# Kernel tuning notes

Measured on AMD Instinct MI355X. Metric: run time of the kernel, lower is better.

Reference implementation:

```python
import jax, jax.numpy as jnp
import numpy as np

FP8_E4M3_MAX = 448.0  # max_value for fp8 e4m3fn in the torch module


def _to_fp8_e4m3(x):
    # round-to-nearest fp8 e4m3fn values, represented back in fp32
    return x.astype(jnp.float8_e4m3fn).astype(jnp.float32)


def setup_inputs() -> dict:
    key = jax.random.key(0)
    k1, k2, k3 = jax.random.split(key, 3)
    B, S, K, N = 4, 2048, 4096, 14336
    x = jax.random.normal(k1, (B, S, K), dtype=jnp.float32)
    # per-tensor scales (QParamsLinear enforces per_tensor qscheme for this path)
    weight_scale = jnp.array([0.01], dtype=jnp.float32)
    input_scale = jnp.array([0.02], dtype=jnp.float32)
    # weight stored in real-quantized fp8 form (values are exact e4m3 lattice points)
    w_fp = jax.random.normal(k2, (N, K), dtype=jnp.float32)
    weight_q = _to_fp8_e4m3(jnp.clip(w_fp / weight_scale, -FP8_E4M3_MAX, FP8_E4M3_MAX))
    bias = jax.random.normal(k3, (N,), dtype=jnp.float32)
    return {"x": x, "weight_q": weight_q, "weight_scale": weight_scale,
            "input_scale": input_scale, "bias": bias}


def reference(x, weight_q, weight_scale, input_scale, bias):
    # Quantize activation: divide by per-tensor scale, clamp to fp8 range, cast to e4m3
    qx = jnp.clip(x / input_scale, -FP8_E4M3_MAX, FP8_E4M3_MAX)
    qx = qx.astype(jnp.float8_e4m3fn).astype(x.dtype)
    # scaled_mm: (qx @ weight_q.T) * (input_scale * weight_scale) + bias
    out = jnp.einsum("bsk,nk->bsn", qx, weight_q.astype(x.dtype))
    out = out * (input_scale * weight_scale)[0] + bias
    return out
```

## Files before the change

### kernel.cpp

```cpp
#include <hip/hip_runtime.h>
#include <stdint.h>

typedef float f32x4  __attribute__((ext_vector_type(4)));
typedef float f32x16 __attribute__((ext_vector_type(16)));
typedef int   i32x4  __attribute__((ext_vector_type(4)));
typedef int   i32x8  __attribute__((ext_vector_type(8)));

constexpr int Mdim = 8192;
constexpr int Ndim = 14336;
constexpr int Kdim = 4096;
constexpr int BM = 256, BN = 256, BK = 64;
constexpr int NT = Kdim / BK;
constexpr uint32_t SLOT = 32768;

#define VMCNT(n) asm volatile("s_waitcnt vmcnt(" #n ")" ::: "memory")
#define LGKM(n)  do { asm volatile("s_waitcnt lgkmcnt(" #n ")" ::: "memory"); \
                      __builtin_amdgcn_sched_barrier(0); } while (0)
#define BARRIER() do { asm volatile("" ::: "memory"); \
                       __builtin_amdgcn_s_barrier(); \
                       asm volatile("" ::: "memory"); } while (0)

__device__ __forceinline__ void gload_lds16(const void* g, void* l) {
  __builtin_amdgcn_global_load_lds(
      (const __attribute__((address_space(1))) unsigned int*)g,
      (__attribute__((address_space(3))) unsigned int*)l, 16, 0, 0);
}

__device__ __forceinline__ i32x4 ldsr128(const uint8_t* p) {
  i32x4 r;
  asm volatile("ds_read_b128 %0, %1"
               : "=v"(r)
               : "v"((const __attribute__((address_space(3))) uint8_t*)p));
  return r;
}

__device__ __forceinline__ i32x8 frag(const uint8_t* tile, int row, int kh) {
  const int p0 = (kh * 32) ^ (((row >> 1) & 3) << 4);
  const uint8_t* rp = tile + row * 64;
  i32x4 lo = ldsr128(rp + p0);
  i32x4 hi = ldsr128(rp + (p0 ^ 16));
  return __builtin_shufflevector(lo, hi, 0, 1, 2, 3, 4, 5, 6, 7);
}

__device__ __forceinline__ f32x16 mx(i32x8 a, i32x8 b, f32x16 c) {
  return __builtin_amdgcn_mfma_scale_f32_32x32x64_f8f6f4(
      a, b, c, 0, 0, 0, 0x7f7f7f7f, 0, 0x7f7f7f7f);
}

__global__ void __launch_bounds__(256) quant_fp8_kernel(
    const float* __restrict__ in, uint8_t* __restrict__ out8,
    const float* __restrict__ scale_ptr, long long n)
{
  const float s = scale_ptr ? scale_ptr[0] : 1.0f;
  const long long nch = n >> 3;
  const long long idx = (long long)blockIdx.x * blockDim.x + threadIdx.x;
  const long long stride = (long long)gridDim.x * blockDim.x;
  for (long long c = idx; c < nch; c += stride) {
    f32x4 v0 = *(const f32x4*)(in + c * 8);
    f32x4 v1 = *(const f32x4*)(in + c * 8 + 4);
    float q[8];
#pragma unroll
    for (int j = 0; j < 4; ++j) {
      q[j]     = fminf(fmaxf(v0[j] / s, -448.f), 448.f);
      q[4 + j] = fminf(fmaxf(v1[j] / s, -448.f), 448.f);
    }
    unsigned int w0 = 0, w1 = 0;
    w0 = __builtin_amdgcn_cvt_pk_fp8_f32(q[0], q[1], w0, false);
    w0 = __builtin_amdgcn_cvt_pk_fp8_f32(q[2], q[3], w0, true);
    w1 = __builtin_amdgcn_cvt_pk_fp8_f32(q[4], q[5], w1, false);
    w1 = __builtin_amdgcn_cvt_pk_fp8_f32(q[6], q[7], w1, true);
    uint2 r; r.x = w0; r.y = w1;
    *(uint2*)(out8 + c * 8) = r;
  }
}

__global__ void __launch_bounds__(512, 2) gemm_fp8_kernel(
    const uint8_t* __restrict__ qa, const uint8_t* __restrict__ qb,
    const float* __restrict__ iscale, const float* __restrict__ wscale,
    const float* __restrict__ bias, float* __restrict__ out)
{
  __shared__ uint8_t smem[4 * SLOT];

  const int tid  = threadIdx.x;
  const int wave = tid >> 6;
  const int lane = tid & 63;
  const int wm   = wave >> 2;
  const int wn   = wave & 3;
  const int col  = lane & 31;
  const int kh   = lane >> 5;
  const long long tile_m = (long long)blockIdx.y * BM;
  const long long tile_n = (long long)blockIdx.x * BN;

  const int urow = tid >> 2;
  const int pbs  = tid & 3;
  const int scol = (pbs ^ ((urow >> 1) & 3)) << 4;
  const uint8_t* gA = qa + (tile_m + urow) * Kdim + scol;
  const uint8_t* gB = qb + (tile_n + urow) * Kdim + scol;
  uint8_t* lbase = smem + wave * 1024;

#define STAGE(u, mat, tt, boff)                                            \
  gload_lds16((mat ? gB : gA) + (long long)(u) * 128 * Kdim +              \
                  (long long)(tt) * BK,                                    \
              lbase + (boff) + (mat) * 16384 + (u) * 8192)

  f32x16 acc[4][2] = {};

  const int rowA = wm * 128 + col;
  const int rowB = wn * 64 + col;

#pragma unroll
  for (int tt = 0; tt < 3; ++tt) {
    STAGE(0, 0, tt, (uint32_t)tt * SLOT); STAGE(1, 0, tt, (uint32_t)tt * SLOT);
    STAGE(0, 1, tt, (uint32_t)tt * SLOT); STAGE(1, 1, tt, (uint32_t)tt * SLOT);
  }

  for (int t = 0; t < NT; ++t) {
    const uint8_t* Ab = smem + (uint32_t)(t & 3) * SLOT;
    const uint8_t* Bb = Ab + 16384;

    if (t + 2 < NT)      { VMCNT(8); }
    else if (t + 1 < NT) { VMCNT(4); }
    else                 { VMCNT(0); }
    BARRIER();

    if (t + 3 < NT) {
      const uint32_t bo = (uint32_t)((t + 3) & 3) * SLOT;
      STAGE(0, 0, t + 3, bo); STAGE(1, 0, t + 3, bo);
      STAGE(0, 1, t + 3, bo); STAGE(1, 1, t + 3, bo);
    }

    i32x8 A0 = frag(Ab, rowA +  0, kh);
    i32x8 A1 = frag(Ab, rowA + 32, kh);
    i32x8 B0 = frag(Bb, rowB +  0, kh);
    i32x8 B1 = frag(Bb, rowB + 32, kh);
    i32x8 A2 = frag(Ab, rowA + 64, kh);
    i32x8 A3 = frag(Ab, rowA + 96, kh);

    LGKM(4);
    __builtin_amdgcn_s_setprio(1);
    acc[0][0] = mx(A0, B0, acc[0][0]);  acc[0][1] = mx(A0, B1, acc[0][1]);
    acc[1][0] = mx(A1, B0, acc[1][0]);  acc[1][1] = mx(A1, B1, acc[1][1]);
    __builtin_amdgcn_s_setprio(0);
    LGKM(0);
    __builtin_amdgcn_s_setprio(1);
    acc[2][0] = mx(A2, B0, acc[2][0]);  acc[2][1] = mx(A2, B1, acc[2][1]);
    acc[3][0] = mx(A3, B0, acc[3][0]);  acc[3][1] = mx(A3, B1, acc[3][1]);
    __builtin_amdgcn_s_setprio(0);
  }

  const float alpha = iscale[0] * wscale[0];
  const long long col0 = tile_n + wn * 64 + col;
  const float bv0 = bias[col0];
  const float bv1 = bias[col0 + 32];
#pragma unroll
  for (int m = 0; m < 4; ++m) {
#pragma unroll
    for (int r = 0; r < 16; ++r) {
      const long long row =
          tile_m + wm * 128 + m * 32 + (r & 3) + 8 * (r >> 2) + 4 * kh;
      float* op = out + row * (long long)Ndim + col0;
      op[0]  = acc[m][0][r] * alpha + bv0;
      op[32] = acc[m][1][r] * alpha + bv1;
    }
  }
#undef STAGE
}

extern "C" void kernel_launch(void* const* d_in, const int* in_sizes, int n_in,
                              void* d_out, int out_size, void* d_ws, size_t ws_size,
                              hipStream_t stream) {
  const float* x      = (const float*)d_in[0];
  const float* weight = (const float*)d_in[1];
  const float* wscale = (const float*)d_in[2];
  const float* iscale = (const float*)d_in[3];
  const float* bias   = (const float*)d_in[4];
  float* out = (float*)d_out;

  uint8_t* qx = (uint8_t*)d_ws;
  uint8_t* qw = qx + (long long)Mdim * Kdim;

  const long long nx = (long long)Mdim * Kdim;
  const long long nw = (long long)Ndim * Kdim;

  quant_fp8_kernel<<<4096, 256, 0, stream>>>(x, qx, iscale, nx);
  quant_fp8_kernel<<<4096, 256, 0, stream>>>(weight, qw, nullptr, nw);

  dim3 grid(Ndim / BN, Mdim / BM);
  gemm_fp8_kernel<<<grid, 512, 0, stream>>>(qx, qw, iscale, wscale, bias, out);
}
```

Measured before the change: 570.2 us.

## Pre-swizzle weights into MFMA fragment layout and load B directly to registers

The weight quantization kernel now writes fp8 weights in a layout pre-arranged per MFMA fragment, so the GEMM loads B operands straight from global memory into registers instead of staging them through LDS. Only A goes through LDS now, with BK raised to 128, a double buffer instead of a 4-stage ring, and a new swizzle. The main loop is unrolled by two, with register double-buffering of the B fragments. This removes LDS traffic and capacity for B, but it gives up the deeper prefetch depth (waits on vmcnt(0) every step) and raises register pressure.

```diff
diff --git a/kernel.cpp b/kernel.cpp
--- a/kernel.cpp
+++ b/kernel.cpp
@@ -1,24 +1,26 @@
 #include <hip/hip_runtime.h>
 #include <stdint.h>
 
-typedef float f32x4  __attribute__((ext_vector_type(4)));
-typedef float f32x16 __attribute__((ext_vector_type(16)));
-typedef int   i32x4  __attribute__((ext_vector_type(4)));
-typedef int   i32x8  __attribute__((ext_vector_type(8)));
+typedef float    f32x4  __attribute__((ext_vector_type(4)));
+typedef float    f32x16 __attribute__((ext_vector_type(16)));
+typedef int      i32x4  __attribute__((ext_vector_type(4)));
+typedef int      i32x8  __attribute__((ext_vector_type(8)));
+typedef uint32_t u32x4  __attribute__((ext_vector_type(4)));
 
 constexpr int Mdim = 8192;
 constexpr int Ndim = 14336;
 constexpr int Kdim = 4096;
-constexpr int BM = 256, BN = 256, BK = 64;
+constexpr int BM = 256, BN = 256, BK = 128;
 constexpr int NT = Kdim / BK;
-constexpr uint32_t SLOT = 32768;
-
-#define VMCNT(n) asm volatile("s_waitcnt vmcnt(" #n ")" ::: "memory")
+
+#define VMCNT(n) do { asm volatile("s_waitcnt vmcnt(" #n ")" ::: "memory"); \
+                      __builtin_amdgcn_sched_barrier(0); } while (0)
 #define LGKM(n)  do { asm volatile("s_waitcnt lgkmcnt(" #n ")" ::: "memory"); \
                       __builtin_amdgcn_sched_barrier(0); } while (0)
 #define BARRIER() do { asm volatile("" ::: "memory"); \
                        __builtin_amdgcn_s_barrier(); \
                        asm volatile("" ::: "memory"); } while (0)
+#define KEEP(x)  asm volatile("" :: "v"(x))
 
 __device__ __forceinline__ void gload_lds16(const void* g, void* l) {
   __builtin_amdgcn_global_load_lds(
@@ -34,9 +36,9 @@
   return r;
 }
 
-__device__ __forceinline__ i32x8 frag(const uint8_t* tile, int row, int kh) {
-  const int p0 = (kh * 32) ^ (((row >> 1) & 3) << 4);
-  const uint8_t* rp = tile + row * 64;
+__device__ __forceinline__ i32x8 frag(const uint8_t* tile, int row, int kb) {
+  const int p0 = kb ^ ((row & 7) << 4);
+  const uint8_t* rp = tile + row * BK;
   i32x4 lo = ldsr128(rp + p0);
   i32x4 hi = ldsr128(rp + (p0 ^ 16));
   return __builtin_shufflevector(lo, hi, 0, 1, 2, 3, 4, 5, 6, 7);
@@ -51,7 +53,7 @@
     const float* __restrict__ in, uint8_t* __restrict__ out8,
     const float* __restrict__ scale_ptr, long long n)
 {
-  const float s = scale_ptr ? scale_ptr[0] : 1.0f;
+  const float s = scale_ptr[0];
   const long long nch = n >> 3;
   const long long idx = (long long)blockIdx.x * blockDim.x + threadIdx.x;
   const long long stride = (long long)gridDim.x * blockDim.x;
@@ -74,12 +76,49 @@
   }
 }
 
+__global__ void __launch_bounds__(256) quant_w_flat_kernel(
+    const float* __restrict__ w, uint8_t* __restrict__ out)
+{
+  __shared__ uint32_t lds[32][260];
+  const int n0  = blockIdx.x >> 2;
+  const int kq  = blockIdx.x & 3;
+  const int tid = threadIdx.x;
+#pragma unroll 4
+  for (int r = 0; r < 32; ++r) {
+    const float* src =
+        w + (long long)(n0 * 32 + r) * Kdim + kq * 1024 + tid * 4;
+    f32x4 v = *(const f32x4*)src;
+    float q0 = fminf(fmaxf(v[0], -448.f), 448.f);
+    float q1 = fminf(fmaxf(v[1], -448.f), 448.f);
+    float q2 = fminf(fmaxf(v[2], -448.f), 448.f);
+    float q3 = fminf(fmaxf(v[3], -448.f), 448.f);
+    unsigned int pk = 0;
+    pk = __builtin_amdgcn_cvt_pk_fp8_f32(q0, q1, pk, false);
+    pk = __builtin_amdgcn_cvt_pk_fp8_f32(q2, q3, pk, true);
+    lds[r][tid] = pk;
+  }
+  __syncthreads();
+#pragma unroll
+  for (int i = 0; i < 4; ++i) {
+    const int it  = i * 256 + tid;
+    const int k0l = it >> 6;
+    const int l   = it & 63;
+    const uint32_t* src = &lds[l & 31][k0l * 16 + (l >> 5) * 8];
+    u32x4 lo = *(const u32x4*)src;
+    u32x4 hi = *(const u32x4*)(src + 4);
+    uint8_t* dst =
+        out + (long long)(n0 * 64 + kq * 16 + k0l) * 2048 + l * 32;
+    *(u32x4*)dst = lo;
+    *(u32x4*)(dst + 16) = hi;
+  }
+}
+
 __global__ void __launch_bounds__(512, 2) gemm_fp8_kernel(
     const uint8_t* __restrict__ qa, const uint8_t* __restrict__ qb,
     const float* __restrict__ iscale, const float* __restrict__ wscale,
     const float* __restrict__ bias, float* __restrict__ out)
 {
-  __shared__ uint8_t smem[4 * SLOT];
+  __shared__ uint8_t smem[2 * 32768];
 
   const int tid  = threadIdx.x;
   const int wave = tid >> 6;
@@ -91,62 +130,94 @@
   const long long tile_m = (long long)blockIdx.y * BM;
   const long long tile_n = (long long)blockIdx.x * BN;
 
-  const int urow = tid >> 2;
-  const int pbs  = tid & 3;
-  const int scol = (pbs ^ ((urow >> 1) & 3)) << 4;
+  const int urow = tid >> 3;
+  const int pbs  = tid & 7;
+  const int scol = (pbs ^ (urow & 7)) << 4;
   const uint8_t* gA = qa + (tile_m + urow) * Kdim + scol;
-  const uint8_t* gB = qb + (tile_n + urow) * Kdim + scol;
   uint8_t* lbase = smem + wave * 1024;
 
-#define STAGE(u, mat, tt, boff)                                            \
-  gload_lds16((mat ? gB : gA) + (long long)(u) * 128 * Kdim +              \
-                  (long long)(tt) * BK,                                    \
-              lbase + (boff) + (mat) * 16384 + (u) * 8192)
+#define STAGE(u, k0, boff)                                                \
+  gload_lds16(gA + (long long)(u) * 64 * Kdim + (k0),                     \
+              lbase + (boff) + (u) * 8192)
+
+  const int n0g0 = (int)(tile_n >> 5) + wn * 2;
+  const uint8_t* pB0 = qb + (long long)n0g0 * 131072 + lane * 32;
+  const uint8_t* pB1 = pB0 + 131072;
 
   f32x16 acc[4][2] = {};
-
   const int rowA = wm * 128 + col;
-  const int rowB = wn * 64 + col;
-
-#pragma unroll
-  for (int tt = 0; tt < 3; ++tt) {
-    STAGE(0, 0, tt, (uint32_t)tt * SLOT); STAGE(1, 0, tt, (uint32_t)tt * SLOT);
-    STAGE(0, 1, tt, (uint32_t)tt * SLOT); STAGE(1, 1, tt, (uint32_t)tt * SLOT);
-  }
-
-  for (int t = 0; t < NT; ++t) {
-    const uint8_t* Ab = smem + (uint32_t)(t & 3) * SLOT;
-    const uint8_t* Bb = Ab + 16384;
-
-    if (t + 2 < NT)      { VMCNT(8); }
-    else if (t + 1 < NT) { VMCNT(4); }
-    else                 { VMCNT(0); }
-    BARRIER();
-
-    if (t + 3 < NT) {
-      const uint32_t bo = (uint32_t)((t + 3) & 3) * SLOT;
-      STAGE(0, 0, t + 3, bo); STAGE(1, 0, t + 3, bo);
-      STAGE(0, 1, t + 3, bo); STAGE(1, 1, t + 3, bo);
-    }
-
-    i32x8 A0 = frag(Ab, rowA +  0, kh);
-    i32x8 A1 = frag(Ab, rowA + 32, kh);
-    i32x8 B0 = frag(Bb, rowB +  0, kh);
-    i32x8 B1 = frag(Bb, rowB + 32, kh);
-    i32x8 A2 = frag(Ab, rowA + 64, kh);
-    i32x8 A3 = frag(Ab, rowA + 96, kh);
-
-    LGKM(4);
-    __builtin_amdgcn_s_setprio(1);
-    acc[0][0] = mx(A0, B0, acc[0][0]);  acc[0][1] = mx(A0, B1, acc[0][1]);
-    acc[1][0] = mx(A1, B0, acc[1][0]);  acc[1][1] = mx(A1, B1, acc[1][1]);
-    __builtin_amdgcn_s_setprio(0);
-    LGKM(0);
-    __builtin_amdgcn_s_setprio(1);
-    acc[2][0] = mx(A2, B0, acc[2][0]);  acc[2][1] = mx(A2, B1, acc[2][1]);
-    acc[3][0] = mx(A3, B0, acc[3][0]);  acc[3][1] = mx(A3, B1, acc[3][1]);
-    __builtin_amdgcn_s_setprio(0);
-  }
+  const int kb0 = kh * 32;
+  const int kb1 = 64 + kh * 32;
+
+#define BODY(T, PF, Bc00, Bc10, Bc01, Bc11, Bn00, Bn10, Bn01, Bn11)          \
+  {                                                                          \
+    const uint8_t* Ab = smem + (((T) & 1) ? 32768u : 0u);                    \
+    VMCNT(0);          \
+    BARRIER();                                \
+    KEEP(Bc00); KEEP(Bc10); KEEP(Bc01); KEEP(Bc11);                          \
+    if (PF) {                                                                \
+      const uint32_t bo = (((T) + 1) & 1) ? 32768u : 0u;                     \
+      const long long kn = (long long)((T) + 1) * BK;                        \
+      STAGE(0, kn, bo); STAGE(1, kn, bo); STAGE(2, kn, bo); STAGE(3, kn, bo);\
+      const int uo = ((T) + 1) * 4096;                                       \
+      Bn00 = *(const i32x8*)(pB0 + uo);                                      \
+      Bn10 = *(const i32x8*)(pB1 + uo);                                      \
+      Bn01 = *(const i32x8*)(pB0 + uo + 2048);                               \
+      Bn11 = *(const i32x8*)(pB1 + uo + 2048);                               \
+    }                                                                        \
+    i32x8 A0 = frag(Ab, rowA +  0, kb0);                                     \
+    i32x8 A1 = frag(Ab, rowA + 32, kb0);                                     \
+    i32x8 A2 = frag(Ab, rowA + 64, kb0);                                     \
+    i32x8 A3 = frag(Ab, rowA + 96, kb0);                                     \
+    LGKM(4);                                                \
+    __builtin_amdgcn_s_setprio(1);                                           \
+    acc[0][0] = mx(A0, Bc00, acc[0][0]);                                     \
+    acc[0][1] = mx(A0, Bc10, acc[0][1]);                                     \
+    acc[1][0] = mx(A1, Bc00, acc[1][0]);                                     \
+    acc[1][1] = mx(A1, Bc10, acc[1][1]);                                     \
+    __builtin_amdgcn_s_setprio(0);                                           \
+    i32x8 A4 = frag(Ab, rowA +  0, kb1);                                     \
+    i32x8 A5 = frag(Ab, rowA + 32, kb1);                                     \
+    LGKM(4);                                                \
+    __builtin_amdgcn_s_setprio(1);                                           \
+    acc[2][0] = mx(A2, Bc00, acc[2][0]);                                     \
+    acc[2][1] = mx(A2, Bc10, acc[2][1]);                                     \
+    acc[3][0] = mx(A3, Bc00, acc[3][0]);                                     \
+    acc[3][1] = mx(A3, Bc10, acc[3][1]);                                     \
+    __builtin_amdgcn_s_setprio(0);                                           \
+    i32x8 A6 = frag(Ab, rowA + 64, kb1);                                     \
+    i32x8 A7 = frag(Ab, rowA + 96, kb1);                                     \
+    LGKM(4);                                                \
+    __builtin_amdgcn_s_setprio(1);                                           \
+    acc[0][0] = mx(A4, Bc01, acc[0][0]);                                     \
+    acc[0][1] = mx(A4, Bc11, acc[0][1]);                                     \
+    acc[1][0] = mx(A5, Bc01, acc[1][0]);                                     \
+    acc[1][1] = mx(A5, Bc11, acc[1][1]);                                     \
+    __builtin_amdgcn_s_setprio(0);                                           \
+    LGKM(0);                       \
+    BARRIER();                 \
+    __builtin_amdgcn_s_setprio(1);                                           \
+    acc[2][0] = mx(A6, Bc01, acc[2][0]);                                     \
+    acc[2][1] = mx(A6, Bc11, acc[2][1]);                                     \
+    acc[3][0] = mx(A7, Bc01, acc[3][0]);                                     \
+    acc[3][1] = mx(A7, Bc11, acc[3][1]);                                     \
+    __builtin_amdgcn_s_setprio(0);                                           \
+  }
+
+  i32x8 Bc00, Bc10, Bc01, Bc11, Bn00, Bn10, Bn01, Bn11;
+
+  STAGE(0, 0, 0); STAGE(1, 0, 0); STAGE(2, 0, 0); STAGE(3, 0, 0);
+  Bc00 = *(const i32x8*)(pB0);
+  Bc10 = *(const i32x8*)(pB1);
+  Bc01 = *(const i32x8*)(pB0 + 2048);
+  Bc11 = *(const i32x8*)(pB1 + 2048);
+
+  for (int t = 0; t < NT - 2; t += 2) {
+    BODY(t,     1, Bc00, Bc10, Bc01, Bc11, Bn00, Bn10, Bn01, Bn11);
+    BODY(t + 1, 1, Bn00, Bn10, Bn01, Bn11, Bc00, Bc10, Bc01, Bc11);
+  }
+  BODY(NT - 2, 1, Bc00, Bc10, Bc01, Bc11, Bn00, Bn10, Bn01, Bn11);
+  BODY(NT - 1, 0, Bn00, Bn10, Bn01, Bn11, Bc00, Bc10, Bc01, Bc11);
 
   const float alpha = iscale[0] * wscale[0];
   const long long col0 = tile_n + wn * 64 + col;
@@ -163,6 +234,7 @@
       op[32] = acc[m][1][r] * alpha + bv1;
     }
   }
+#undef BODY
 #undef STAGE
 }
 
@@ -176,15 +248,14 @@
   const float* bias   = (const float*)d_in[4];
   float* out = (float*)d_out;
 
-  uint8_t* qx = (uint8_t*)d_ws;
-  uint8_t* qw = qx + (long long)Mdim * Kdim;
+  uint8_t* qx  = (uint8_t*)d_ws;
+  uint8_t* qb2 = qx + (long long)Mdim * Kdim;
 
   const long long nx = (long long)Mdim * Kdim;
-  const long long nw = (long long)Ndim * Kdim;
 
   quant_fp8_kernel<<<4096, 256, 0, stream>>>(x, qx, iscale, nx);
-  quant_fp8_kernel<<<4096, 256, 0, stream>>>(weight, qw, nullptr, nw);
+  quant_w_flat_kernel<<<(Ndim / 32) * 4, 256, 0, stream>>>(weight, qb2);
 
   dim3 grid(Ndim / BN, Mdim / BM);
-  gemm_fp8_kernel<<<grid, 512, 0, stream>>>(qx, qw, iscale, wscale, bias, out);
-}
+  gemm_fp8_kernel<<<grid, 512, 0, stream>>>(qx, qb2, iscale, wscale, bias, out);
+}
```

Result: slower. 635.8 us (+11.5%).
